# Kernel optimization log

Measured on AMD Instinct MI355X. Metric: run time of the kernel, lower is better.

The kernel has to match this reference:

```python
import jax, jax.numpy as jnp
import numpy as np

N, SD, VD, LD = 8192, 512, 4096, 768
TAU = 0.5
K = 6    # topk over stru->mm similarity
K2 = 6   # topk2 over mm->mm similarity
BN_EPS = 1e-5
LRELU_SLOPE = 0.01


def _mlp_bn(x, W1, b1, W2, b2, gamma, beta):
    # Linear -> LeakyReLU -> Linear -> BatchNorm1d (training mode, batch stats)
    h = x @ W1 + b1
    h = jnp.where(h >= 0, h, LRELU_SLOPE * h)
    h = h @ W2 + b2
    mu = h.mean(axis=0)
    var = h.var(axis=0)  # biased variance, as torch BN uses for normalization
    return (h - mu) / jnp.sqrt(var + BN_EPS) * gamma + beta


def _cossim(x, y):
    xn = x / (jnp.linalg.norm(x, axis=-1, keepdims=True) + 1e-12)
    yn = y / (jnp.linalg.norm(y, axis=-1, keepdims=True) + 1e-12)
    return xn @ yn.T


def _neibor_mnce_v2(stru, mm):
    sm = jnp.exp(_cossim(stru, mm) / TAU)   # [N, N]
    mmd = _cossim(mm, mm)                    # [N, N]
    _, maxSM = jax.lax.top_k(sm, K)          # [N, K]
    rows = jnp.arange(stru.shape[0])[:, None]
    pos = []
    for i in range(K):  # fixed small loop over topk columns (as in original)
        idx = maxSM[:, i]                         # [N]
        _, mm_idx = jax.lax.top_k(mmd[idx], K2)   # gather rows then topk -> [N, K2]
        pos.append(sm[rows, mm_idx])              # [N, K2]
    pos = jnp.concatenate(pos, axis=-1)           # [N, K*K2]
    return jnp.mean(-jnp.log(pos.sum(-1) / sm.sum(-1)))


def setup_inputs() -> dict:
    key = jax.random.key(0)
    ks = jax.random.split(key, 11)
    d = {
        'stru_feats': jax.random.normal(ks[0], (N, SD), jnp.float32),
        'visu_feats': jax.random.normal(ks[1], (N, VD), jnp.float32),
        'ling_feats': jax.random.normal(ks[2], (N, LD), jnp.float32),
        # fusion_l_vl params
        'Wl1': jax.random.normal(ks[3], (LD, SD), jnp.float32) / np.sqrt(LD),
        'bl1': jnp.zeros((SD,), jnp.float32),
        'Wl2': jax.random.normal(ks[4], (SD, SD), jnp.float32) / np.sqrt(SD),
        'bl2': jnp.zeros((SD,), jnp.float32),
        'gl': jnp.ones((SD,), jnp.float32),
        'betal': jnp.zeros((SD,), jnp.float32),
        # fusion_v_vl params
        'Wv1': jax.random.normal(ks[5], (VD, SD), jnp.float32) / np.sqrt(VD),
        'bv1': jnp.zeros((SD,), jnp.float32),
        'Wv2': jax.random.normal(ks[6], (SD, SD), jnp.float32) / np.sqrt(SD),
        'bv2': jnp.zeros((SD,), jnp.float32),
        'gv': jnp.ones((SD,), jnp.float32),
        'betav': jnp.zeros((SD,), jnp.float32),
    }
    return d


def reference(stru_feats, visu_feats, ling_feats,
              Wl1, bl1, Wl2, bl2, gl, betal,
              Wv1, bv1, Wv2, bv2, gv, betav):
    ling = _mlp_bn(ling_feats, Wl1, bl1, Wl2, bl2, gl, betal)
    visu = _mlp_bn(visu_feats, Wv1, bv1, Wv2, bv2, gv, betav)
    loss_sl = _neibor_mnce_v2(stru_feats, ling)
    loss_sv = _neibor_mnce_v2(stru_feats, visu)
    return (loss_sl + loss_sv, ling, visu)
```

## Files before the change

### kernel.cpp

```cpp
#include <hip/hip_runtime.h>
#include <hip/hip_bf16.h>
#include <math.h>

typedef __bf16 bf16;
typedef __attribute__((ext_vector_type(8))) __bf16 bf16x8;
typedef __attribute__((ext_vector_type(4))) float floatx4;

static_assert(sizeof(bf16x8) == 16, "bf16x8 must be 16B");

__global__ void row_normalize_kernel(const float* __restrict__ x, bf16* __restrict__ out) {
  __shared__ float red[256];
  int row = blockIdx.x;
  int t = threadIdx.x;
  float v0 = x[(size_t)row * 512 + t];
  float v1 = x[(size_t)row * 512 + t + 256];
  red[t] = v0 * v0 + v1 * v1;
  __syncthreads();
  for (int d = 128; d > 0; d >>= 1) {
    if (t < d) red[t] += red[t + d];
    __syncthreads();
  }
  float scale = 1.0f / (sqrtf(red[0]) + 1e-12f);
  out[(size_t)row * 512 + t] = (bf16)(v0 * scale);
  out[(size_t)row * 512 + t + 256] = (bf16)(v1 * scale);
}

__global__ void cast_bf16_kernel(const float* __restrict__ x, bf16* __restrict__ out, long n) {
  long i = ((long)blockIdx.x * blockDim.x + threadIdx.x) * 8;
  long stride = (long)gridDim.x * blockDim.x * 8;
  for (; i < n; i += stride) {
    floatx4 a = *(const floatx4*)(x + i);
    floatx4 b = *(const floatx4*)(x + i + 4);
    bf16x8 v;
#pragma unroll
    for (int e = 0; e < 4; ++e) v[e] = (bf16)a[e];
#pragma unroll
    for (int e = 0; e < 4; ++e) v[e + 4] = (bf16)b[e];
    *(bf16x8*)(out + i) = v;
  }
}

__global__ void transpose_cast_kernel(const float* __restrict__ W, bf16* __restrict__ Wt, int K) {
  __shared__ float t[64][65];
  int k0 = blockIdx.x * 64;
  int n0 = blockIdx.y * 64;
#pragma unroll
  for (int m = 0; m < 16; ++m) {
    int kk = (threadIdx.x >> 6) + m * 4;
    int nn = threadIdx.x & 63;
    t[kk][nn] = W[(size_t)(k0 + kk) * 512 + n0 + nn];
  }
  __syncthreads();
#pragma unroll
  for (int m = 0; m < 16; ++m) {
    int nn = (threadIdx.x >> 6) + m * 4;
    int kk = threadIdx.x & 63;
    Wt[(size_t)(n0 + nn) * K + k0 + kk] = (bf16)t[kk][nn];
  }
}

__global__ void bn_stats_kernel(const float* __restrict__ h, float* __restrict__ colsum,
                                float* __restrict__ colsumsq) {
  int col = threadIdx.x;
  int r0 = blockIdx.x * 32;
  float s = 0.f, s2 = 0.f;
  for (int r = r0; r < r0 + 32; ++r) {
    float v = h[(size_t)r * 512 + col];
    s += v;
    s2 += v * v;
  }
  atomicAdd(&colsum[col], s);
  atomicAdd(&colsumsq[col], s2);
}

__global__ void bn_apply_kernel(const float* __restrict__ h, const float* __restrict__ colsum,
                                const float* __restrict__ colsumsq, const float* __restrict__ gamma,
                                const float* __restrict__ beta, float* __restrict__ mm_out,
                                bf16* __restrict__ mmn) {
  __shared__ float red[512];
  int row = blockIdx.x, col = threadIdx.x;
  float mean = colsum[col] * (1.0f / 8192.0f);
  float var = colsumsq[col] * (1.0f / 8192.0f) - mean * mean;
  float inv = rsqrtf(var + 1e-5f);
  float y = (h[(size_t)row * 512 + col] - mean) * inv * gamma[col] + beta[col];
  mm_out[(size_t)row * 512 + col] = y;
  red[col] = y * y;
  __syncthreads();
  for (int d = 256; d > 0; d >>= 1) {
    if (col < d) red[col] += red[col + d];
    __syncthreads();
  }
  float scale = 1.0f / (sqrtf(red[0]) + 1e-12f);
  mmn[(size_t)row * 512 + col] = (bf16)(y * scale);
}

template <int MODE, bool AF32>
__launch_bounds__(256, 2) __global__
void gemm_nt_kernel(const void* __restrict__ Av, const bf16* __restrict__ B,
                    const float* __restrict__ bias, bf16* __restrict__ out_bf,
                    float* __restrict__ out_f, int K) {
  __shared__ __align__(16) bf16 As[2][128][64];
  __shared__ __align__(16) bf16 Bs[2][64][64];

  const int tid = threadIdx.x;
  const int lane = tid & 63;
  const int wave = tid >> 6;
  const int q = lane >> 4;
  const int ml = lane & 15;
  const int row0 = blockIdx.x * 128;
  const int col0 = blockIdx.y * 64;

  const float* Af = (const float*)Av;
  const bf16* Ab = (const bf16*)Av;

  const int sr = tid >> 3;
  const int sc = tid & 7;

  floatx4 acc[2][4];
#pragma unroll
  for (int g = 0; g < 2; ++g)
#pragma unroll
    for (int f = 0; f < 4; ++f) acc[g][f] = (floatx4)0.0f;

  {
#pragma unroll
    for (int m = 0; m < 4; ++m) {
      int r = sr + m * 32;
      bf16x8 v;
      if constexpr (AF32) {
        const float* p = Af + (size_t)(row0 + r) * K + sc * 8;
#pragma unroll
        for (int e = 0; e < 8; ++e) v[e] = (bf16)p[e];
      } else {
        v = *(const bf16x8*)(Ab + (size_t)(row0 + r) * K + sc * 8);
      }
      *(bf16x8*)&As[0][r][(sc ^ (r & 7)) * 8] = v;
    }
#pragma unroll
    for (int m = 0; m < 2; ++m) {
      int r = sr + m * 32;
      *(bf16x8*)&Bs[0][r][(sc ^ (r & 7)) * 8] =
          *(const bf16x8*)(B + (size_t)(col0 + r) * K + sc * 8);
    }
  }

  const int nsteps = K >> 6;
  int buf = 0;
  for (int s = 0; s < nsteps; ++s) {
    __syncthreads();
    const bool has_next = (s + 1) < nsteps;
    floatx4 af[4][2];
    bf16x8 ab[4];
    bf16x8 bb[2];
    if (has_next) {
      const int kt = (s + 1) << 6;
#pragma unroll
      for (int m = 0; m < 4; ++m) {
        if constexpr (AF32) {
          const floatx4* p = (const floatx4*)(Af + (size_t)(row0 + sr + m * 32) * K + kt + sc * 8);
          af[m][0] = p[0];
          af[m][1] = p[1];
        } else {
          ab[m] = *(const bf16x8*)(Ab + (size_t)(row0 + sr + m * 32) * K + kt + sc * 8);
        }
      }
#pragma unroll
      for (int m = 0; m < 2; ++m)
        bb[m] = *(const bf16x8*)(B + (size_t)(col0 + sr + m * 32) * K + kt + sc * 8);
    }
#pragma unroll
    for (int kh = 0; kh < 2; ++kh) {
      const int slot = ((q + kh * 4) ^ (ml & 7)) * 8;
      bf16x8 a0 = *(const bf16x8*)&As[buf][wave * 32 + ml][slot];
      bf16x8 a1 = *(const bf16x8*)&As[buf][wave * 32 + 16 + ml][slot];
#pragma unroll
      for (int f = 0; f < 4; ++f) {
        bf16x8 b = *(const bf16x8*)&Bs[buf][f * 16 + ml][slot];
        acc[0][f] = __builtin_amdgcn_mfma_f32_16x16x32_bf16(a0, b, acc[0][f], 0, 0, 0);
        acc[1][f] = __builtin_amdgcn_mfma_f32_16x16x32_bf16(a1, b, acc[1][f], 0, 0, 0);
      }
    }
    if (has_next) {
#pragma unroll
      for (int m = 0; m < 4; ++m) {
        int r = sr + m * 32;
        bf16x8 v;
        if constexpr (AF32) {
#pragma unroll
          for (int e = 0; e < 8; ++e) v[e] = (bf16)af[m][e >> 2][e & 3];
        } else {
          v = ab[m];
        }
        *(bf16x8*)&As[buf ^ 1][r][(sc ^ (r & 7)) * 8] = v;
      }
#pragma unroll
      for (int m = 0; m < 2; ++m) {
        int r = sr + m * 32;
        *(bf16x8*)&Bs[buf ^ 1][r][(sc ^ (r & 7)) * 8] = bb[m];
      }
    }
    buf ^= 1;
  }

#pragma unroll
  for (int f = 0; f < 4; ++f) {
    int colg = col0 + f * 16 + ml;
    float bv = bias[colg];
#pragma unroll
    for (int g = 0; g < 2; ++g)
#pragma unroll
      for (int i = 0; i < 4; ++i) {
        int rowg = row0 + wave * 32 + g * 16 + q * 4 + i;
        float v = acc[g][f][i] + bv;
        if constexpr (MODE == 0) {
          v = v >= 0.f ? v : 0.01f * v;
          out_bf[(size_t)rowg * 512 + colg] = (bf16)v;
        } else {
          out_f[(size_t)rowg * 512 + colg] = v;
        }
      }
  }
}

__device__ __forceinline__ unsigned pack_key(float v, int col) {
  unsigned u = __float_as_uint(v);
  u = (u & 0x80000000u) ? ~u : (u | 0x80000000u);
  return (u & 0xFFFFE000u) | (unsigned)(8191 - col);
}

#define NPARTS 8

__launch_bounds__(256, 2) __global__
void topk_sm_fused_kernel(const bf16* __restrict__ Amm, const bf16* __restrict__ Ast,
                          const bf16* __restrict__ B, unsigned* __restrict__ keys_mm,
                          unsigned* __restrict__ keys_sm, float* __restrict__ rowsum_part) {
  __shared__ __align__(16) bf16 Bs[2][64][128];

  const int tid = threadIdx.x;
  const int lane = tid & 63;
  const int wave = tid >> 6;
  const int q = lane >> 4;
  const int ml = lane & 15;
  const int row0 = blockIdx.x * 64;
  const int part = blockIdx.y;

  const int str = tid >> 4;
  const int scu = tid & 15;
  const int ssc = scu ^ str;

  bf16x8 afr[2][16];
#pragma unroll
  for (int g = 0; g < 2; ++g) {
    const bf16* ap = (g == 0 ? Amm : Ast) + (size_t)(row0 + wave * 16 + ml) * 512 + q * 8;
#pragma unroll
    for (int s = 0; s < 16; ++s) afr[g][s] = *(const bf16x8*)(ap + s * 32);
  }

  unsigned p6[2][4][6];
#pragma unroll
  for (int g = 0; g < 2; ++g)
#pragma unroll
    for (int i = 0; i < 4; ++i)
#pragma unroll
      for (int j = 0; j < 6; ++j) p6[g][i][j] = 0u;
  float srow[4] = {0.f, 0.f, 0.f, 0.f};

  int buf = 0;
  {
    const bf16* bp = B + (size_t)(part * 1024 + str) * 512 + scu * 8;
#pragma unroll
    for (int m = 0; m < 4; ++m)
      *(bf16x8*)&Bs[0][str + m * 16][ssc * 8] = *(const bf16x8*)(bp + (size_t)m * 16 * 512);
  }

  for (int ct = 0; ct < 16; ++ct) {
    const int col0 = part * 1024 + ct * 64;
    floatx4 acc[2][4];
#pragma unroll
    for (int g = 0; g < 2; ++g)
#pragma unroll
      for (int f = 0; f < 4; ++f) acc[g][f] = (floatx4)0.0f;

#pragma unroll
    for (int kt4 = 0; kt4 < 4; ++kt4) {
      __syncthreads();
      bf16x8 st[4];
      const bool has_next = !(ct == 15 && kt4 == 3);
      if (has_next) {
        const int nct = (kt4 == 3) ? ct + 1 : ct;
        const int nk = (kt4 == 3) ? 0 : (kt4 + 1) * 128;
        const bf16* bp = B + (size_t)(part * 1024 + nct * 64 + str) * 512 + nk + scu * 8;
#pragma unroll
        for (int m = 0; m < 4; ++m) st[m] = *(const bf16x8*)(bp + (size_t)m * 16 * 512);
      }
#pragma unroll
      for (int kk2 = 0; kk2 < 4; ++kk2) {
#pragma unroll
        for (int f = 0; f < 4; ++f) {
          const int sc2 = (kk2 * 4 + q) ^ ml;
          bf16x8 b = *(const bf16x8*)&Bs[buf][f * 16 + ml][sc2 * 8];
          acc[0][f] = __builtin_amdgcn_mfma_f32_16x16x32_bf16(afr[0][kt4 * 4 + kk2], b, acc[0][f], 0, 0, 0);
          acc[1][f] = __builtin_amdgcn_mfma_f32_16x16x32_bf16(afr[1][kt4 * 4 + kk2], b, acc[1][f], 0, 0, 0);
        }
      }
      if (has_next) {
#pragma unroll
        for (int m = 0; m < 4; ++m)
          *(bf16x8*)&Bs[buf ^ 1][str + m * 16][ssc * 8] = st[m];
      }
      buf ^= 1;
    }

#pragma unroll
    for (int i = 0; i < 4; ++i) {
      float s = 0.f;
#pragma unroll
      for (int f = 0; f < 4; ++f) s += __expf(2.0f * acc[1][f][i]);
      srow[i] += s;
#pragma unroll
      for (int g = 0; g < 2; ++g)
#pragma unroll
        for (int f = 0; f < 4; ++f) {
          unsigned key = pack_key(acc[g][f][i], col0 + f * 16 + ml);
          if (key > p6[g][i][5]) {
#pragma unroll
            for (int j = 5; j >= 1; --j) {
              bool ap = key > p6[g][i][j - 1];
              unsigned keep = (key > p6[g][i][j]) ? key : p6[g][i][j];
              p6[g][i][j] = ap ? p6[g][i][j - 1] : keep;
            }
            if (key > p6[g][i][0]) p6[g][i][0] = key;
          }
        }
    }
  }

#pragma unroll
  for (int i = 0; i < 4; ++i) {
    const int lrow = wave * 16 + q * 4 + i;
    {
      float s = srow[i];
      s += __shfl_xor(s, 1);
      s += __shfl_xor(s, 2);
      s += __shfl_xor(s, 4);
      s += __shfl_xor(s, 8);
      if (ml == 0) rowsum_part[(size_t)(row0 + lrow) * NPARTS + part] = s;
    }
#pragma unroll
    for (int g = 0; g < 2; ++g) {
      unsigned* dk = g ? keys_sm : keys_mm;
      const size_t o = ((size_t)(row0 + lrow) * NPARTS + part) * 6;
#pragma unroll
      for (int k = 0; k < 6; ++k) {
        unsigned mk = p6[g][i][0];
#pragma unroll
        for (int d = 1; d < 16; d <<= 1) {
          unsigned ok = (unsigned)__shfl_xor((int)mk, d);
          if (ok > mk) mk = ok;
        }
        if (ml == 0) dk[o + k] = mk;
        if (p6[g][i][0] == mk) {
#pragma unroll
          for (int j = 0; j < 5; ++j) p6[g][i][j] = p6[g][i][j + 1];
          p6[g][i][5] = 0u;
        }
      }
    }
  }
}

__global__ void merge_top6_kernel(const unsigned* __restrict__ part_keys,
                                  int* __restrict__ out_idx,
                                  const float* __restrict__ rowsum_part, float* __restrict__ rowsum,
                                  int do_rowsum) {
  int row = blockIdx.x * blockDim.x + threadIdx.x;
  if (row >= 8192) return;
  unsigned best[6] = {0u, 0u, 0u, 0u, 0u, 0u};
  for (int p = 0; p < NPARTS; ++p) {
#pragma unroll
    for (int c = 0; c < 6; ++c) {
      unsigned k = part_keys[((size_t)row * NPARTS + p) * 6 + c];
      if (k > best[5]) {
#pragma unroll
        for (int j = 5; j >= 1; --j) {
          bool ap = k > best[j - 1];
          unsigned keep = (k > best[j]) ? k : best[j];
          best[j] = ap ? best[j - 1] : keep;
        }
        if (k > best[0]) best[0] = k;
      }
    }
  }
#pragma unroll
  for (int j = 0; j < 6; ++j) out_idx[row * 6 + j] = 8191 - (int)(best[j] & 0x1FFFu);
  if (do_rowsum) {
    float s = 0.f;
    for (int p = 0; p < NPARTS; ++p) s += rowsum_part[(size_t)row * NPARTS + p];
    rowsum[row] = s;
  }
}

__global__ void loss_kernel(const bf16* __restrict__ strun, const bf16* __restrict__ mmn,
                            const int* __restrict__ top6, const int* __restrict__ nbr,
                            const float* __restrict__ rowsum, float* __restrict__ out0) {
  int w = (int)((blockIdx.x * blockDim.x + threadIdx.x) >> 6);
  int lane = threadIdx.x & 63;
  if (w >= 8192) return;
  bf16x8 sv = *(const bf16x8*)(strun + (size_t)w * 512 + lane * 8);
  float sf[8];
#pragma unroll
  for (int e = 0; e < 8; ++e) sf[e] = (float)sv[e];
  float pos = 0.f;
  for (int k = 0; k < 6; ++k) {
    int j = top6[w * 6 + k];
#pragma unroll
    for (int l = 0; l < 6; ++l) {
      int m = nbr[j * 6 + l];
      bf16x8 mv = *(const bf16x8*)(mmn + (size_t)m * 512 + lane * 8);
      float d = 0.f;
#pragma unroll
      for (int e = 0; e < 8; ++e) d += sf[e] * (float)mv[e];
      d += __shfl_xor(d, 1);
      d += __shfl_xor(d, 2);
      d += __shfl_xor(d, 4);
      d += __shfl_xor(d, 8);
      d += __shfl_xor(d, 16);
      d += __shfl_xor(d, 32);
      pos += __expf(2.0f * d);
    }
  }
  if (lane == 0) {
    float loss_r = logf(rowsum[w]) - logf(pos);
    atomicAdd(out0, loss_r * (1.0f / 8192.0f));
  }
}

extern "C" void kernel_launch(void* const* d_in, const int* in_sizes, int n_in, void* d_out,
                              int out_size, void* d_ws, size_t ws_size, hipStream_t stream) {
  const float* stru = (const float*)d_in[0];
  const float* visu = (const float*)d_in[1];
  const float* ling = (const float*)d_in[2];
  const float* Wl1 = (const float*)d_in[3];
  const float* bl1 = (const float*)d_in[4];
  const float* Wl2 = (const float*)d_in[5];
  const float* bl2 = (const float*)d_in[6];
  const float* gl = (const float*)d_in[7];
  const float* betal = (const float*)d_in[8];
  const float* Wv1 = (const float*)d_in[9];
  const float* bv1 = (const float*)d_in[10];
  const float* Wv2 = (const float*)d_in[11];
  const float* bv2 = (const float*)d_in[12];
  const float* gv = (const float*)d_in[13];
  const float* betav = (const float*)d_in[14];
  float* out = (float*)d_out;

  char* p = (char*)d_ws;
  auto alloc = [&](size_t bytes) {
    char* r = p;
    p += (bytes + 255) & ~(size_t)255;
    return r;
  };
  bf16* strun = (bf16*)alloc((size_t)8192 * 512 * 2);
  bf16* W1t = (bf16*)alloc((size_t)512 * 4096 * 2);
  bf16* W2t = (bf16*)alloc((size_t)512 * 512 * 2);
  bf16* H1 = (bf16*)alloc((size_t)8192 * 512 * 2);
  float* H2 = (float*)alloc((size_t)8192 * 512 * 4);
  bf16* mmn = (bf16*)alloc((size_t)8192 * 512 * 2);
  float* colsum = (float*)alloc(512 * 4);
  float* colsumsq = (float*)alloc(512 * 4);
  float* rowsum_part = (float*)alloc((size_t)8192 * NPARTS * 4);
  float* rowsum = (float*)alloc((size_t)8192 * 4);
  unsigned* keys_mm = (unsigned*)alloc((size_t)8192 * NPARTS * 6 * 4);
  unsigned* keys_sm = (unsigned*)alloc((size_t)8192 * NPARTS * 6 * 4);
  int* nbr = (int*)alloc((size_t)8192 * 6 * 4);
  int* top6 = (int*)alloc((size_t)8192 * 6 * 4);

  size_t xb_bytes = (size_t)8192 * 4096 * 2;
  size_t used = (size_t)(p - (char*)d_ws);
  bf16* Xb = nullptr;
  if (used + xb_bytes <= ws_size) Xb = (bf16*)alloc(xb_bytes);

  hipMemsetAsync(d_out, 0, 4, stream);
  row_normalize_kernel<<<8192, 256, 0, stream>>>(stru, strun);

  for (int br = 0; br < 2; ++br) {
    const float* X = (br == 0) ? ling : visu;
    int Kin = (br == 0) ? 768 : 4096;
    const float* W1 = (br == 0) ? Wl1 : Wv1;
    const float* b1 = (br == 0) ? bl1 : bv1;
    const float* W2 = (br == 0) ? Wl2 : Wv2;
    const float* b2 = (br == 0) ? bl2 : bv2;
    const float* g = (br == 0) ? gl : gv;
    const float* bet = (br == 0) ? betal : betav;
    float* mm_out = out + 1 + (size_t)br * 8192 * 512;

    transpose_cast_kernel<<<dim3(Kin / 64, 8), 256, 0, stream>>>(W1, W1t, Kin);
    transpose_cast_kernel<<<dim3(8, 8), 256, 0, stream>>>(W2, W2t, 512);

    if (Xb) {
      cast_bf16_kernel<<<2048, 256, 0, stream>>>(X, Xb, (long)8192 * Kin);
      gemm_nt_kernel<0, false><<<dim3(64, 8), 256, 0, stream>>>(
          Xb, W1t, b1, H1, nullptr, Kin);
    } else {
      gemm_nt_kernel<0, true><<<dim3(64, 8), 256, 0, stream>>>(
          X, W1t, b1, H1, nullptr, Kin);
    }
    gemm_nt_kernel<1, false><<<dim3(64, 8), 256, 0, stream>>>(
        H1, W2t, b2, nullptr, H2, 512);

    hipMemsetAsync(colsum, 0, 512 * 4, stream);
    hipMemsetAsync(colsumsq, 0, 512 * 4, stream);
    bn_stats_kernel<<<256, 512, 0, stream>>>(H2, colsum, colsumsq);
    bn_apply_kernel<<<8192, 512, 0, stream>>>(H2, colsum, colsumsq, g, bet, mm_out, mmn);

    topk_sm_fused_kernel<<<dim3(128, NPARTS), 256, 0, stream>>>(
        mmn, strun, mmn, keys_mm, keys_sm, rowsum_part);
    merge_top6_kernel<<<32, 256, 0, stream>>>(keys_mm, nbr, nullptr, nullptr, 0);
    merge_top6_kernel<<<32, 256, 0, stream>>>(keys_sm, top6, rowsum_part, rowsum, 1);

    loss_kernel<<<2048, 256, 0, stream>>>(strun, mmn, top6, nbr, rowsum, out);
  }
}
```

Measured before the change: 1.116 ms.

## Stage GEMM and top-k B tiles with direct global-to-LDS async loads

Replaces register-staged global loads followed by LDS stores with __builtin_amdgcn_global_load_lds in the bf16 GEMM path and in the fused top-k similarity kernel. The XOR swizzle moves to the global-address side so the LDS layout stays the same. MFMA sections are wrapped in s_setprio to favour issuing matrix instructions. The aim is to remove the VGPR round-trip and LDS write instructions and let the next tile's loads overlap compute. In exchange, the fp32-input GEMM path loses its double buffering and now does load-then-compute with two barriers per step, which may slow the large first MLP layer.

New measurement: 1.071 ms. -4.1%, faster.

```diff
diff --git a/kernel.cpp b/kernel.cpp
--- a/kernel.cpp
+++ b/kernel.cpp
@@ -7,6 +7,11 @@
 typedef __attribute__((ext_vector_type(4))) float floatx4;
 
 static_assert(sizeof(bf16x8) == 16, "bf16x8 must be 16B");
+
+__device__ __forceinline__ void gld16(bf16* lds, const bf16* g) {
+  __builtin_amdgcn_global_load_lds((const __attribute__((address_space(1))) void*)g,
+                                   (__attribute__((address_space(3))) void*)lds, 16, 0, 0);
+}
 
 __global__ void row_normalize_kernel(const float* __restrict__ x, bf16* __restrict__ out) {
   __shared__ float red[256];
@@ -113,93 +118,94 @@
   const float* Af = (const float*)Av;
   const bf16* Ab = (const bf16*)Av;
 
-  const int sr = tid >> 3;
-  const int sc = tid & 7;
-
   floatx4 acc[2][4];
 #pragma unroll
   for (int g = 0; g < 2; ++g)
 #pragma unroll
     for (int f = 0; f < 4; ++f) acc[g][f] = (floatx4)0.0f;
 
-  {
-#pragma unroll
-    for (int m = 0; m < 4; ++m) {
-      int r = sr + m * 32;
-      bf16x8 v;
-      if constexpr (AF32) {
-        const float* p = Af + (size_t)(row0 + r) * K + sc * 8;
-#pragma unroll
-        for (int e = 0; e < 8; ++e) v[e] = (bf16)p[e];
-      } else {
-        v = *(const bf16x8*)(Ab + (size_t)(row0 + r) * K + sc * 8);
-      }
-      *(bf16x8*)&As[0][r][(sc ^ (r & 7)) * 8] = v;
-    }
-#pragma unroll
-    for (int m = 0; m < 2; ++m) {
-      int r = sr + m * 32;
-      *(bf16x8*)&Bs[0][r][(sc ^ (r & 7)) * 8] =
-          *(const bf16x8*)(B + (size_t)(col0 + r) * K + sc * 8);
-    }
-  }
-
   const int nsteps = K >> 6;
-  int buf = 0;
-  for (int s = 0; s < nsteps; ++s) {
-    __syncthreads();
-    const bool has_next = (s + 1) < nsteps;
-    floatx4 af[4][2];
-    bf16x8 ab[4];
-    bf16x8 bb[2];
-    if (has_next) {
-      const int kt = (s + 1) << 6;
+
+  if constexpr (!AF32) {
+    const int grow = lane >> 3;
+    const int gch = (lane & 7) ^ grow;
+
+    auto stageA = [&](int s, int b) {
+      const int kt = s << 6;
 #pragma unroll
       for (int m = 0; m < 4; ++m) {
-        if constexpr (AF32) {
-          const floatx4* p = (const floatx4*)(Af + (size_t)(row0 + sr + m * 32) * K + kt + sc * 8);
-          af[m][0] = p[0];
-          af[m][1] = p[1];
-        } else {
-          ab[m] = *(const bf16x8*)(Ab + (size_t)(row0 + sr + m * 32) * K + kt + sc * 8);
-        }
-      }
-#pragma unroll
-      for (int m = 0; m < 2; ++m)
-        bb[m] = *(const bf16x8*)(B + (size_t)(col0 + sr + m * 32) * K + kt + sc * 8);
-    }
-#pragma unroll
-    for (int kh = 0; kh < 2; ++kh) {
-      const int slot = ((q + kh * 4) ^ (ml & 7)) * 8;
-      bf16x8 a0 = *(const bf16x8*)&As[buf][wave * 32 + ml][slot];
-      bf16x8 a1 = *(const bf16x8*)&As[buf][wave * 32 + 16 + ml][slot];
-#pragma unroll
-      for (int f = 0; f < 4; ++f) {
-        bf16x8 b = *(const bf16x8*)&Bs[buf][f * 16 + ml][slot];
-        acc[0][f] = __builtin_amdgcn_mfma_f32_16x16x32_bf16(a0, b, acc[0][f], 0, 0, 0);
-        acc[1][f] = __builtin_amdgcn_mfma_f32_16x16x32_bf16(a1, b, acc[1][f], 0, 0, 0);
-      }
-    }
-    if (has_next) {
+        const int rb = m * 32 + wave * 8;
+        gld16(&As[b][rb][0], Ab + (size_t)(row0 + rb + grow) * K + kt + gch * 8);
+      }
+    };
+    auto stageB = [&](int s, int b) {
+      const int kt = s << 6;
+#pragma unroll
+      for (int m = 0; m < 2; ++m) {
+        const int rb = m * 32 + wave * 8;
+        gld16(&Bs[b][rb][0], B + (size_t)(col0 + rb + grow) * K + kt + gch * 8);
+      }
+    };
+
+    stageA(0, 0);
+    stageB(0, 0);
+    for (int s = 0; s < nsteps; ++s) {
+      const int b = s & 1;
+      __syncthreads();
+      if (s + 1 < nsteps) {
+        stageA(s + 1, b ^ 1);
+        stageB(s + 1, b ^ 1);
+      }
+      __builtin_amdgcn_s_setprio(1);
+#pragma unroll
+      for (int kh = 0; kh < 2; ++kh) {
+        const int slot = ((q + kh * 4) ^ (ml & 7)) * 8;
+        bf16x8 a0 = *(const bf16x8*)&As[b][wave * 32 + ml][slot];
+        bf16x8 a1 = *(const bf16x8*)&As[b][wave * 32 + 16 + ml][slot];
+#pragma unroll
+        for (int f = 0; f < 4; ++f) {
+          bf16x8 bb = *(const bf16x8*)&Bs[b][f * 16 + ml][slot];
+          acc[0][f] = __builtin_amdgcn_mfma_f32_16x16x32_bf16(a0, bb, acc[0][f], 0, 0, 0);
+          acc[1][f] = __builtin_amdgcn_mfma_f32_16x16x32_bf16(a1, bb, acc[1][f], 0, 0, 0);
+        }
+      }
+      __builtin_amdgcn_s_setprio(0);
+    }
+  } else {
+    const int sr = tid >> 3;
+    const int sc = tid & 7;
+    for (int s = 0; s < nsteps; ++s) {
+      const int kt = s << 6;
+      __syncthreads();
 #pragma unroll
       for (int m = 0; m < 4; ++m) {
         int r = sr + m * 32;
+        const float* pp = Af + (size_t)(row0 + r) * K + kt + sc * 8;
         bf16x8 v;
-        if constexpr (AF32) {
-#pragma unroll
-          for (int e = 0; e < 8; ++e) v[e] = (bf16)af[m][e >> 2][e & 3];
-        } else {
-          v = ab[m];
-        }
-        *(bf16x8*)&As[buf ^ 1][r][(sc ^ (r & 7)) * 8] = v;
+#pragma unroll
+        for (int e = 0; e < 8; ++e) v[e] = (bf16)pp[e];
+        *(bf16x8*)&As[0][r][(sc ^ (r & 7)) * 8] = v;
       }
 #pragma unroll
       for (int m = 0; m < 2; ++m) {
         int r = sr + m * 32;
-        *(bf16x8*)&Bs[buf ^ 1][r][(sc ^ (r & 7)) * 8] = bb[m];
-      }
-    }
-    buf ^= 1;
+        *(bf16x8*)&Bs[0][r][(sc ^ (r & 7)) * 8] =
+            *(const bf16x8*)(B + (size_t)(col0 + r) * K + kt + sc * 8);
+      }
+      __syncthreads();
+#pragma unroll
+      for (int kh = 0; kh < 2; ++kh) {
+        const int slot = ((q + kh * 4) ^ (ml & 7)) * 8;
+        bf16x8 a0 = *(const bf16x8*)&As[0][wave * 32 + ml][slot];
+        bf16x8 a1 = *(const bf16x8*)&As[0][wave * 32 + 16 + ml][slot];
+#pragma unroll
+        for (int f = 0; f < 4; ++f) {
+          bf16x8 bb = *(const bf16x8*)&Bs[0][f * 16 + ml][slot];
+          acc[0][f] = __builtin_amdgcn_mfma_f32_16x16x32_bf16(a0, bb, acc[0][f], 0, 0, 0);
+          acc[1][f] = __builtin_amdgcn_mfma_f32_16x16x32_bf16(a1, bb, acc[1][f], 0, 0, 0);
+        }
+      }
+    }
   }
 
 #pragma unroll
@@ -244,9 +250,8 @@
   const int row0 = blockIdx.x * 64;
   const int part = blockIdx.y;
 
-  const int str = tid >> 4;
-  const int scu = tid & 15;
-  const int ssc = scu ^ str;
+  const int strw = wave * 4 + (lane >> 4);
+  const int gch = (lane & 15) ^ strw;
 
   bf16x8 afr[2][16];
 #pragma unroll
@@ -265,13 +270,15 @@
       for (int j = 0; j < 6; ++j) p6[g][i][j] = 0u;
   float srow[4] = {0.f, 0.f, 0.f, 0.f};
 
-  int buf = 0;
-  {
-    const bf16* bp = B + (size_t)(part * 1024 + str) * 512 + scu * 8;
+  auto stage = [&](int u, int b) {
+    const bf16* bp =
+        B + (size_t)(part * 1024 + (u >> 2) * 64 + strw) * 512 + (u & 3) * 128 + gch * 8;
 #pragma unroll
     for (int m = 0; m < 4; ++m)
-      *(bf16x8*)&Bs[0][str + m * 16][ssc * 8] = *(const bf16x8*)(bp + (size_t)m * 16 * 512);
-  }
+      gld16(&Bs[b][wave * 4 + m * 16][0], bp + (size_t)m * 16 * 512);
+  };
+
+  stage(0, 0);
 
   for (int ct = 0; ct < 16; ++ct) {
     const int col0 = part * 1024 + ct * 64;
@@ -283,32 +290,21 @@
 
 #pragma unroll
     for (int kt4 = 0; kt4 < 4; ++kt4) {
+      const int t = ct * 4 + kt4;
       __syncthreads();
-      bf16x8 st[4];
-      const bool has_next = !(ct == 15 && kt4 == 3);
-      if (has_next) {
-        const int nct = (kt4 == 3) ? ct + 1 : ct;
-        const int nk = (kt4 == 3) ? 0 : (kt4 + 1) * 128;
-        const bf16* bp = B + (size_t)(part * 1024 + nct * 64 + str) * 512 + nk + scu * 8;
-#pragma unroll
-        for (int m = 0; m < 4; ++m) st[m] = *(const bf16x8*)(bp + (size_t)m * 16 * 512);
-      }
+      if (t < 63) stage(t + 1, (t + 1) & 1);
+      __builtin_amdgcn_s_setprio(1);
 #pragma unroll
       for (int kk2 = 0; kk2 < 4; ++kk2) {
 #pragma unroll
         for (int f = 0; f < 4; ++f) {
           const int sc2 = (kk2 * 4 + q) ^ ml;
-          bf16x8 b = *(const bf16x8*)&Bs[buf][f * 16 + ml][sc2 * 8];
+          bf16x8 b = *(const bf16x8*)&Bs[t & 1][f * 16 + ml][sc2 * 8];
           acc[0][f] = __builtin_amdgcn_mfma_f32_16x16x32_bf16(afr[0][kt4 * 4 + kk2], b, acc[0][f], 0, 0, 0);
           acc[1][f] = __builtin_amdgcn_mfma_f32_16x16x32_bf16(afr[1][kt4 * 4 + kk2], b, acc[1][f], 0, 0, 0);
         }
       }
-      if (has_next) {
-#pragma unroll
-        for (int m = 0; m < 4; ++m)
-          *(bf16x8*)&Bs[buf ^ 1][str + m * 16][ssc * 8] = st[m];
-      }
-      buf ^= 1;
+      __builtin_amdgcn_s_setprio(0);
     }
 
 #pragma unroll
```
